# Kernel optimization log

Measured on AMD Instinct MI355X. Metric: run time of the kernel, lower is better.

## Reference

```python
import jax, jax.numpy as jnp
import numpy as np

N = 4096
D = 512
H = 3


def setup_inputs() -> dict:
    key = jax.random.key(0)
    k1, k2, k3 = jax.random.split(key, 3)
    graph_info = (jax.random.uniform(k1, (N, N)) < 0.01).astype(jnp.float32)
    h = jax.random.normal(k2, (N, D), dtype=jnp.float32)
    # xavier_normal_ with relu gain: std = sqrt(2) * sqrt(2/(fan_in+fan_out))
    std = np.sqrt(2.0) * np.sqrt(2.0 / (D + H))
    P = jax.random.normal(k3, (D, H), dtype=jnp.float32) * jnp.float32(std)
    return {"graph_info": graph_info, "h": h, "P": P}


def reference(graph_info, h, P):
    # graph_info_1 = spmm(graph_info^T, I)^T == graph_info (identity densification)
    mask = graph_info > 0                                  # [N, N]
    E = jax.nn.relu(h @ P)                                 # [N, H] per-node scores, all heads
    NEG = jnp.float32(-9e15)
    # e is broadcast along rows: att[i, j] = E[j, k] where edge (i->j) exists
    logits = jnp.where(mask[None, :, :], E.T[:, None, :], NEG)  # [H, N, N]
    att = jax.nn.softmax(logits, axis=-1)                  # row-softmax per head
    hh = jnp.einsum('hij,jd->hid', att, h)                 # [H, N, D] aggregate
    # sum_flag == 1: scale each row i by its degree (rowsum of graph_info_1)
    rowsum = jnp.sum(graph_info, axis=-1)                  # [N]
    hh = hh * rowsum[None, :, None]
    # multi_head > 1, concat=False: sum over heads
    return jnp.sum(hh, axis=0)                             # [N, D]
```

## Files before the change

### kernel.cpp

```cpp
#include <hip/hip_runtime.h>
#include <stdint.h>

#define NN 4096
#define DD 512
#define NH 3
#define WMAX 64

__device__ __forceinline__ unsigned short f2bf_rn(float x) {
    union { float f; uint32_t u; } v; v.f = x;
    uint32_t u = v.u;
    uint32_t r = (u + 0x7FFFu + ((u >> 16) & 1u)) >> 16;
    return (unsigned short)r;
}
__device__ __forceinline__ float bflo(uint32_t u) {
    union { uint32_t u; float f; } v; v.u = u << 16; return v.f;
}
__device__ __forceinline__ float bfhi(uint32_t u) {
    union { uint32_t u; float f; } v; v.u = u & 0xFFFF0000u; return v.f;
}

__global__ __launch_bounds__(256) void prep_kernel(
    const float* __restrict__ h, const float* __restrict__ P,
    float* __restrict__ w, unsigned short* __restrict__ hb)
{
    int gid = blockIdx.x * 256 + threadIdx.x;
    int row = gid >> 6, ln = gid & 63;
    const float4* h4 = (const float4*)(h + (size_t)row * DD);
    float4 va = h4[ln * 2], vb = h4[ln * 2 + 1];
    float e[8] = { va.x, va.y, va.z, va.w, vb.x, vb.y, vb.z, vb.w };

    uint32_t pk0 = (uint32_t)f2bf_rn(e[0]) | ((uint32_t)f2bf_rn(e[1]) << 16);
    uint32_t pk1 = (uint32_t)f2bf_rn(e[2]) | ((uint32_t)f2bf_rn(e[3]) << 16);
    uint32_t pk2 = (uint32_t)f2bf_rn(e[4]) | ((uint32_t)f2bf_rn(e[5]) << 16);
    uint32_t pk3 = (uint32_t)f2bf_rn(e[6]) | ((uint32_t)f2bf_rn(e[7]) << 16);
    *(uint4*)(hb + (size_t)row * DD + ln * 8) = make_uint4(pk0, pk1, pk2, pk3);

    int d0 = ln * 8;
    float a0 = 0.f, a1 = 0.f, a2 = 0.f;
    #pragma unroll
    for (int k = 0; k < 8; ++k) {
        float hv = e[k];
        const float* Pr = P + (size_t)(d0 + k) * NH;
        a0 = fmaf(hv, Pr[0], a0);
        a1 = fmaf(hv, Pr[1], a1);
        a2 = fmaf(hv, Pr[2], a2);
    }
    #pragma unroll
    for (int off = 32; off > 0; off >>= 1) {
        a0 += __shfl_down(a0, off);
        a1 += __shfl_down(a1, off);
        a2 += __shfl_down(a2, off);
    }
    if (ln == 0) {
        w[row * NH + 0] = expf(fmaxf(a0, 0.f));
        w[row * NH + 1] = expf(fmaxf(a1, 0.f));
        w[row * NH + 2] = expf(fmaxf(a2, 0.f));
    }
}

__global__ __launch_bounds__(256) void att_agg_kernel(
    const float* __restrict__ g, const unsigned short* __restrict__ hb,
    const float* __restrict__ w, float* __restrict__ out)
{
    __shared__ float s_part[4 * NH * DD];
    __shared__ int   s_list[4 * WMAX];
    __shared__ float s_z[4][NH];
    __shared__ int   s_cw[4];

    const int row = blockIdx.x, tid = threadIdx.x;
    const int wv = tid >> 6, ln = tid & 63;

    const float4* g4 = (const float4*)(g + (size_t)row * NN) + wv * 256;
    float4 v0 = g4[ln], v1 = g4[64 + ln], v2 = g4[128 + ln], v3 = g4[192 + ln];

    int* mylist = s_list + wv * WMAX;
    int cbase = wv * 1024;
    int cnt = 0;
    float4 vs[4] = { v0, v1, v2, v3 };
    #pragma unroll
    for (int k = 0; k < 4; ++k) {
        float comp[4] = { vs[k].x, vs[k].y, vs[k].z, vs[k].w };
        int col0 = cbase + k * 256 + ln * 4;
        #pragma unroll
        for (int c = 0; c < 4; ++c) {
            bool p = comp[c] > 0.f;
            unsigned long long m = __ballot(p);
            if (p) {
                unsigned pre = __builtin_amdgcn_mbcnt_lo((unsigned)m, 0u);
                pre = __builtin_amdgcn_mbcnt_hi((unsigned)(m >> 32), pre);
                int pos = cnt + (int)pre;
                if (pos < WMAX) mylist[pos] = col0 + c;
            }
            cnt += __popcll(m);
        }
    }
    if (cnt > WMAX) cnt = WMAX;

    float accA[8] = {0,0,0,0,0,0,0,0};
    float accB[8] = {0,0,0,0,0,0,0,0};
    float accC[8] = {0,0,0,0,0,0,0,0};
    float z0 = 0.f, z1 = 0.f, z2 = 0.f;
    const unsigned short* hcol = hb + ln * 8;

    if (cnt > 0) {
        int j = mylist[0];
        uint4 rn = *(const uint4*)(hcol + (size_t)j * DD);
        const float* wr = w + (size_t)j * NH;
        float wn0 = wr[0], wn1 = wr[1], wn2 = wr[2];
        for (int t = 0; t < cnt; ++t) {
            uint4 r = rn;
            float c0 = wn0, c1 = wn1, c2 = wn2;
            if (t + 1 < cnt) {
                int j2 = mylist[t + 1];
                rn = *(const uint4*)(hcol + (size_t)j2 * DD);
                const float* wr2 = w + (size_t)j2 * NH;
                wn0 = wr2[0]; wn1 = wr2[1]; wn2 = wr2[2];
            }
            z0 += c0; z1 += c1; z2 += c2;
            float e[8] = { bflo(r.x), bfhi(r.x), bflo(r.y), bfhi(r.y),
                           bflo(r.z), bfhi(r.z), bflo(r.w), bfhi(r.w) };
            #pragma unroll
            for (int q = 0; q < 8; ++q) {
                accA[q] = fmaf(c0, e[q], accA[q]);
                accB[q] = fmaf(c1, e[q], accB[q]);
                accC[q] = fmaf(c2, e[q], accC[q]);
            }
        }
    }

    {
        float* base = s_part + (wv * NH + 0) * DD + ln * 8;
        *(float4*)(base)     = make_float4(accA[0], accA[1], accA[2], accA[3]);
        *(float4*)(base + 4) = make_float4(accA[4], accA[5], accA[6], accA[7]);
        base = s_part + (wv * NH + 1) * DD + ln * 8;
        *(float4*)(base)     = make_float4(accB[0], accB[1], accB[2], accB[3]);
        *(float4*)(base + 4) = make_float4(accB[4], accB[5], accB[6], accB[7]);
        base = s_part + (wv * NH + 2) * DD + ln * 8;
        *(float4*)(base)     = make_float4(accC[0], accC[1], accC[2], accC[3]);
        *(float4*)(base + 4) = make_float4(accC[4], accC[5], accC[6], accC[7]);
    }
    if (ln == 0) { s_z[wv][0] = z0; s_z[wv][1] = z1; s_z[wv][2] = z2; s_cw[wv] = cnt; }
    __syncthreads();

    float Z0 = s_z[0][0] + s_z[1][0] + s_z[2][0] + s_z[3][0];
    float Z1 = s_z[0][1] + s_z[1][1] + s_z[2][1] + s_z[3][1];
    float Z2 = s_z[0][2] + s_z[1][2] + s_z[2][2] + s_z[3][2];
    int nnz = s_cw[0] + s_cw[1] + s_cw[2] + s_cw[3];

    int c0 = tid * 2;
    float sA0 = 0.f, sA1 = 0.f, sB0 = 0.f, sB1 = 0.f, sC0 = 0.f, sC1 = 0.f;
    #pragma unroll
    for (int W = 0; W < 4; ++W) {
        float2 pa = *(const float2*)(s_part + (W * NH + 0) * DD + c0);
        float2 pb = *(const float2*)(s_part + (W * NH + 1) * DD + c0);
        float2 pc = *(const float2*)(s_part + (W * NH + 2) * DD + c0);
        sA0 += pa.x; sA1 += pa.y;
        sB0 += pb.x; sB1 += pb.y;
        sC0 += pc.x; sC1 += pc.y;
    }
    float2 res;
    if (nnz == 0) {
        res = make_float2(0.f, 0.f);
    } else {
        float rs = (float)nnz;
        float i0 = rs / Z0, i1 = rs / Z1, i2 = rs / Z2;
        res.x = fmaf(sA0, i0, fmaf(sB0, i1, sC0 * i2));
        res.y = fmaf(sA1, i0, fmaf(sB1, i1, sC1 * i2));
    }
    ((float2*)(out + (size_t)row * DD))[tid] = res;
}

extern "C" void kernel_launch(void* const* d_in, const int* in_sizes, int n_in,
                              void* d_out, int out_size, void* d_ws, size_t ws_size,
                              hipStream_t stream) {
    const float* g = (const float*)d_in[0];
    const float* h = (const float*)d_in[1];
    const float* P = (const float*)d_in[2];
    float* out = (float*)d_out;

    float* w           = (float*)d_ws;
    unsigned short* hb = (unsigned short*)((char*)d_ws + (64 << 10));

    prep_kernel<<<(NN * 64) / 256, 256, 0, stream>>>(h, P, w, hb);
    att_agg_kernel<<<NN, 256, 0, stream>>>(g, hb, w, out);
}
```

Before: 118.0 us.

## Use nontemporal loads/stores, deepen gather prefetch, halve LDS reduction buffer

Streams the dense adjacency rows, the h input and the output through nontemporal loads and stores so they do not pollute cache meant for the gathered bf16 rows. The neighbor gather loop now prefetches two rows ahead instead of one, to hide more global-load latency. The cross-wave partial reduction uses half the LDS: waves 2-3 add into the buffers written by waves 0-1, which lowers LDS footprint and may raise occupancy but costs an extra barrier.

```diff
diff --git a/kernel.cpp b/kernel.cpp
--- a/kernel.cpp
+++ b/kernel.cpp
@@ -5,6 +5,10 @@
 #define DD 512
 #define NH 3
 #define WMAX 64
+
+typedef float        f32x4 __attribute__((ext_vector_type(4)));
+typedef float        f32x2 __attribute__((ext_vector_type(2)));
+typedef unsigned int u32x4 __attribute__((ext_vector_type(4)));
 
 __device__ __forceinline__ unsigned short f2bf_rn(float x) {
     union { float f; uint32_t u; } v; v.f = x;
@@ -25,15 +29,17 @@
 {
     int gid = blockIdx.x * 256 + threadIdx.x;
     int row = gid >> 6, ln = gid & 63;
-    const float4* h4 = (const float4*)(h + (size_t)row * DD);
-    float4 va = h4[ln * 2], vb = h4[ln * 2 + 1];
+    const f32x4* h4 = (const f32x4*)(h + (size_t)row * DD);
+    f32x4 va = __builtin_nontemporal_load(h4 + ln * 2);
+    f32x4 vb = __builtin_nontemporal_load(h4 + ln * 2 + 1);
     float e[8] = { va.x, va.y, va.z, va.w, vb.x, vb.y, vb.z, vb.w };
 
     uint32_t pk0 = (uint32_t)f2bf_rn(e[0]) | ((uint32_t)f2bf_rn(e[1]) << 16);
     uint32_t pk1 = (uint32_t)f2bf_rn(e[2]) | ((uint32_t)f2bf_rn(e[3]) << 16);
     uint32_t pk2 = (uint32_t)f2bf_rn(e[4]) | ((uint32_t)f2bf_rn(e[5]) << 16);
     uint32_t pk3 = (uint32_t)f2bf_rn(e[6]) | ((uint32_t)f2bf_rn(e[7]) << 16);
-    *(uint4*)(hb + (size_t)row * DD + ln * 8) = make_uint4(pk0, pk1, pk2, pk3);
+    u32x4 pk; pk.x = pk0; pk.y = pk1; pk.z = pk2; pk.w = pk3;
+    *(u32x4*)(hb + (size_t)row * DD + ln * 8) = pk;
 
     int d0 = ln * 8;
     float a0 = 0.f, a1 = 0.f, a2 = 0.f;
@@ -62,7 +68,7 @@
     const float* __restrict__ g, const unsigned short* __restrict__ hb,
     const float* __restrict__ w, float* __restrict__ out)
 {
-    __shared__ float s_part[4 * NH * DD];
+    __shared__ float s_part[2 * NH * DD];
     __shared__ int   s_list[4 * WMAX];
     __shared__ float s_z[4][NH];
     __shared__ int   s_cw[4];
@@ -70,13 +76,16 @@
     const int row = blockIdx.x, tid = threadIdx.x;
     const int wv = tid >> 6, ln = tid & 63;
 
-    const float4* g4 = (const float4*)(g + (size_t)row * NN) + wv * 256;
-    float4 v0 = g4[ln], v1 = g4[64 + ln], v2 = g4[128 + ln], v3 = g4[192 + ln];
+    const f32x4* g4 = (const f32x4*)(g + (size_t)row * NN) + wv * 256;
+    f32x4 v0 = __builtin_nontemporal_load(g4 + ln);
+    f32x4 v1 = __builtin_nontemporal_load(g4 + 64 + ln);
+    f32x4 v2 = __builtin_nontemporal_load(g4 + 128 + ln);
+    f32x4 v3 = __builtin_nontemporal_load(g4 + 192 + ln);
 
     int* mylist = s_list + wv * WMAX;
     int cbase = wv * 1024;
     int cnt = 0;
-    float4 vs[4] = { v0, v1, v2, v3 };
+    f32x4 vs[4] = { v0, v1, v2, v3 };
     #pragma unroll
     for (int k = 0; k < 4; ++k) {
         float comp[4] = { vs[k].x, vs[k].y, vs[k].z, vs[k].w };
@@ -102,33 +111,43 @@
     float z0 = 0.f, z1 = 0.f, z2 = 0.f;
     const unsigned short* hcol = hb + ln * 8;
 
+    u32x4 r0, r1;
+    float wa0 = 0.f, wa1 = 0.f, wa2 = 0.f, wb0 = 0.f, wb1 = 0.f, wb2 = 0.f;
     if (cnt > 0) {
         int j = mylist[0];
-        uint4 rn = *(const uint4*)(hcol + (size_t)j * DD);
+        r0 = *(const u32x4*)(hcol + (size_t)j * DD);
         const float* wr = w + (size_t)j * NH;
-        float wn0 = wr[0], wn1 = wr[1], wn2 = wr[2];
-        for (int t = 0; t < cnt; ++t) {
-            uint4 r = rn;
-            float c0 = wn0, c1 = wn1, c2 = wn2;
-            if (t + 1 < cnt) {
-                int j2 = mylist[t + 1];
-                rn = *(const uint4*)(hcol + (size_t)j2 * DD);
-                const float* wr2 = w + (size_t)j2 * NH;
-                wn0 = wr2[0]; wn1 = wr2[1]; wn2 = wr2[2];
-            }
-            z0 += c0; z1 += c1; z2 += c2;
-            float e[8] = { bflo(r.x), bfhi(r.x), bflo(r.y), bfhi(r.y),
-                           bflo(r.z), bfhi(r.z), bflo(r.w), bfhi(r.w) };
-            #pragma unroll
-            for (int q = 0; q < 8; ++q) {
-                accA[q] = fmaf(c0, e[q], accA[q]);
-                accB[q] = fmaf(c1, e[q], accB[q]);
-                accC[q] = fmaf(c2, e[q], accC[q]);
-            }
+        wa0 = wr[0]; wa1 = wr[1]; wa2 = wr[2];
+    }
+    if (cnt > 1) {
+        int j = mylist[1];
+        r1 = *(const u32x4*)(hcol + (size_t)j * DD);
+        const float* wr = w + (size_t)j * NH;
+        wb0 = wr[0]; wb1 = wr[1]; wb2 = wr[2];
+    }
+    for (int t = 0; t < cnt; ++t) {
+        u32x4 r = r0;
+        float c0 = wa0, c1 = wa1, c2 = wa2;
+        r0 = r1; wa0 = wb0; wa1 = wb1; wa2 = wb2;
+        if (t + 2 < cnt) {
+            int j2 = mylist[t + 2];
+            r1 = *(const u32x4*)(hcol + (size_t)j2 * DD);
+            const float* wr2 = w + (size_t)j2 * NH;
+            wb0 = wr2[0]; wb1 = wr2[1]; wb2 = wr2[2];
         }
-    }
-
-    {
+        z0 += c0; z1 += c1; z2 += c2;
+        float e[8] = { bflo(r.x), bfhi(r.x), bflo(r.y), bfhi(r.y),
+                       bflo(r.z), bfhi(r.z), bflo(r.w), bfhi(r.w) };
+        #pragma unroll
+        for (int q = 0; q < 8; ++q) {
+            accA[q] = fmaf(c0, e[q], accA[q]);
+            accB[q] = fmaf(c1, e[q], accB[q]);
+            accC[q] = fmaf(c2, e[q], accC[q]);
+        }
+    }
+
+    if (ln == 0) { s_z[wv][0] = z0; s_z[wv][1] = z1; s_z[wv][2] = z2; s_cw[wv] = cnt; }
+    if (wv < 2) {
         float* base = s_part + (wv * NH + 0) * DD + ln * 8;
         *(float4*)(base)     = make_float4(accA[0], accA[1], accA[2], accA[3]);
         *(float4*)(base + 4) = make_float4(accA[4], accA[5], accA[6], accA[7]);
@@ -139,7 +158,24 @@
         *(float4*)(base)     = make_float4(accC[0], accC[1], accC[2], accC[3]);
         *(float4*)(base + 4) = make_float4(accC[4], accC[5], accC[6], accC[7]);
     }
-    if (ln == 0) { s_z[wv][0] = z0; s_z[wv][1] = z1; s_z[wv][2] = z2; s_cw[wv] = cnt; }
+    __syncthreads();
+    if (wv >= 2) {
+        float* base = s_part + ((wv - 2) * NH + 0) * DD + ln * 8;
+        float4 p0 = *(float4*)(base), p1 = *(float4*)(base + 4);
+        p0.x += accA[0]; p0.y += accA[1]; p0.z += accA[2]; p0.w += accA[3];
+        p1.x += accA[4]; p1.y += accA[5]; p1.z += accA[6]; p1.w += accA[7];
+        *(float4*)(base) = p0; *(float4*)(base + 4) = p1;
+        base = s_part + ((wv - 2) * NH + 1) * DD + ln * 8;
+        p0 = *(float4*)(base); p1 = *(float4*)(base + 4);
+        p0.x += accB[0]; p0.y += accB[1]; p0.z += accB[2]; p0.w += accB[3];
+        p1.x += accB[4]; p1.y += accB[5]; p1.z += accB[6]; p1.w += accB[7];
+        *(float4*)(base) = p0; *(float4*)(base + 4) = p1;
+        base = s_part + ((wv - 2) * NH + 2) * DD + ln * 8;
+        p0 = *(float4*)(base); p1 = *(float4*)(base + 4);
+        p0.x += accC[0]; p0.y += accC[1]; p0.z += accC[2]; p0.w += accC[3];
+        p1.x += accC[4]; p1.y += accC[5]; p1.z += accC[6]; p1.w += accC[7];
+        *(float4*)(base) = p0; *(float4*)(base + 4) = p1;
+    }
     __syncthreads();
 
     float Z0 = s_z[0][0] + s_z[1][0] + s_z[2][0] + s_z[3][0];
@@ -150,7 +186,7 @@
     int c0 = tid * 2;
     float sA0 = 0.f, sA1 = 0.f, sB0 = 0.f, sB1 = 0.f, sC0 = 0.f, sC1 = 0.f;
     #pragma unroll
-    for (int W = 0; W < 4; ++W) {
+    for (int W = 0; W < 2; ++W) {
         float2 pa = *(const float2*)(s_part + (W * NH + 0) * DD + c0);
         float2 pb = *(const float2*)(s_part + (W * NH + 1) * DD + c0);
         float2 pc = *(const float2*)(s_part + (W * NH + 2) * DD + c0);
@@ -158,16 +194,16 @@
         sB0 += pb.x; sB1 += pb.y;
         sC0 += pc.x; sC1 += pc.y;
     }
-    float2 res;
+    f32x2 res;
     if (nnz == 0) {
-        res = make_float2(0.f, 0.f);
+        res.x = 0.f; res.y = 0.f;
     } else {
         float rs = (float)nnz;
         float i0 = rs / Z0, i1 = rs / Z1, i2 = rs / Z2;
         res.x = fmaf(sA0, i0, fmaf(sB0, i1, sC0 * i2));
         res.y = fmaf(sA1, i0, fmaf(sB1, i1, sC1 * i2));
     }
-    ((float2*)(out + (size_t)row * DD))[tid] = res;
+    __builtin_nontemporal_store(res, (f32x2*)(out + (size_t)row * DD) + tid);
 }
 
 extern "C" void kernel_launch(void* const* d_in, const int* in_sizes, int n_in,
```

Result: slower. 124.1 us (+5.2%).

## Move adjacency scan into prep kernel as bitmask, one wave per row in aggregation

Applied to the files above, without the earlier changes.

The dense adjacency scan now runs in the prep kernel, which compresses each row into 64 bitmask words using non-temporal loads. Those blocks run concurrently with the h-to-bf16 conversion blocks in the same launch. The aggregation kernel reads the compact bitmask and builds the neighbour list with a prefix scan, processing one row per wavefront. This removes the cross-wave shared-memory reduction and uses a two-deep prefetch of neighbour rows. The changes raise the neighbour cap to 128 and shorten the dependency chain, but each wave now walks its row's whole neighbour list serially.

```diff
diff --git a/kernel.cpp b/kernel.cpp
--- a/kernel.cpp
+++ b/kernel.cpp
@@ -4,7 +4,10 @@
 #define NN 4096
 #define DD 512
 #define NH 3
-#define WMAX 64
+#define WMAX 128
+
+typedef float        f32x4 __attribute__((ext_vector_type(4)));
+typedef unsigned int u32x4 __attribute__((ext_vector_type(4)));
 
 __device__ __forceinline__ unsigned short f2bf_rn(float x) {
     union { float f; uint32_t u; } v; v.f = x;
@@ -19,21 +22,48 @@
     union { uint32_t u; float f; } v; v.u = u & 0xFFFF0000u; return v.f;
 }
 
-__global__ __launch_bounds__(256) void prep_kernel(
-    const float* __restrict__ h, const float* __restrict__ P,
-    float* __restrict__ w, unsigned short* __restrict__ hb)
+__global__ __launch_bounds__(256) void prep_scan_kernel(
+    const float* __restrict__ g, const float* __restrict__ h,
+    const float* __restrict__ P, float* __restrict__ w,
+    unsigned short* __restrict__ hb, unsigned long long* __restrict__ bits)
 {
-    int gid = blockIdx.x * 256 + threadIdx.x;
+    const int b = blockIdx.x;
+    const int tid = threadIdx.x;
+    if (b < NN) {
+        const int row = b, wv = tid >> 6, ln = tid & 63;
+        const f32x4* g4 = (const f32x4*)(g + (size_t)row * NN);
+        f32x4 v[4];
+        #pragma unroll
+        for (int it = 0; it < 4; ++it)
+            v[it] = __builtin_nontemporal_load(g4 + it * 256 + tid);
+        #pragma unroll
+        for (int it = 0; it < 4; ++it) {
+            int chunk = it * 4 + wv;
+            unsigned long long m0 = __ballot(v[it].x > 0.f);
+            unsigned long long m1 = __ballot(v[it].y > 0.f);
+            unsigned long long m2 = __ballot(v[it].z > 0.f);
+            unsigned long long m3 = __ballot(v[it].w > 0.f);
+            if (ln < 4) {
+                unsigned long long ms = (ln == 0) ? m0 : (ln == 1) ? m1
+                                       : (ln == 2) ? m2 : m3;
+                bits[(size_t)row * 64 + chunk * 4 + ln] = ms;
+            }
+        }
+        return;
+    }
+    int gid = (b - NN) * 256 + tid;
     int row = gid >> 6, ln = gid & 63;
-    const float4* h4 = (const float4*)(h + (size_t)row * DD);
-    float4 va = h4[ln * 2], vb = h4[ln * 2 + 1];
+    const f32x4* h4 = (const f32x4*)(h + (size_t)row * DD);
+    f32x4 va = __builtin_nontemporal_load(h4 + ln * 2);
+    f32x4 vb = __builtin_nontemporal_load(h4 + ln * 2 + 1);
     float e[8] = { va.x, va.y, va.z, va.w, vb.x, vb.y, vb.z, vb.w };
 
-    uint32_t pk0 = (uint32_t)f2bf_rn(e[0]) | ((uint32_t)f2bf_rn(e[1]) << 16);
-    uint32_t pk1 = (uint32_t)f2bf_rn(e[2]) | ((uint32_t)f2bf_rn(e[3]) << 16);
-    uint32_t pk2 = (uint32_t)f2bf_rn(e[4]) | ((uint32_t)f2bf_rn(e[5]) << 16);
-    uint32_t pk3 = (uint32_t)f2bf_rn(e[6]) | ((uint32_t)f2bf_rn(e[7]) << 16);
-    *(uint4*)(hb + (size_t)row * DD + ln * 8) = make_uint4(pk0, pk1, pk2, pk3);
+    u32x4 pk;
+    pk.x = (uint32_t)f2bf_rn(e[0]) | ((uint32_t)f2bf_rn(e[1]) << 16);
+    pk.y = (uint32_t)f2bf_rn(e[2]) | ((uint32_t)f2bf_rn(e[3]) << 16);
+    pk.z = (uint32_t)f2bf_rn(e[4]) | ((uint32_t)f2bf_rn(e[5]) << 16);
+    pk.w = (uint32_t)f2bf_rn(e[6]) | ((uint32_t)f2bf_rn(e[7]) << 16);
+    *(u32x4*)(hb + (size_t)row * DD + ln * 8) = pk;
 
     int d0 = ln * 8;
     float a0 = 0.f, a1 = 0.f, a2 = 0.f;
@@ -58,43 +88,41 @@
     }
 }
 
-__global__ __launch_bounds__(256) void att_agg_kernel(
-    const float* __restrict__ g, const unsigned short* __restrict__ hb,
-    const float* __restrict__ w, float* __restrict__ out)
+__global__ __launch_bounds__(256) void agg_kernel(
+    const unsigned long long* __restrict__ bits,
+    const unsigned short* __restrict__ hb, const float* __restrict__ w,
+    float* __restrict__ out)
 {
-    __shared__ float s_part[4 * NH * DD];
-    __shared__ int   s_list[4 * WMAX];
-    __shared__ float s_z[4][NH];
-    __shared__ int   s_cw[4];
+    __shared__ int s_list[4][WMAX];
+    const int tid = threadIdx.x, wv = tid >> 6, ln = tid & 63;
+    const int row = blockIdx.x * 4 + wv;
 
-    const int row = blockIdx.x, tid = threadIdx.x;
-    const int wv = tid >> 6, ln = tid & 63;
+    unsigned long long W = bits[(size_t)row * 64 + ln];
+    int cnt = __popcll(W);
+    int inc = cnt;
+    #pragma unroll
+    for (int d = 1; d < 64; d <<= 1) {
+        int n = __shfl_up(inc, d);
+        if (ln >= d) inc += n;
+    }
+    int nnz = __shfl(inc, 63);
+    int o = inc - cnt;
+    int base_col = (ln >> 2) * 256 + (ln & 3);
+    unsigned long long Wt = W;
+    while (Wt) {
+        int bp = __builtin_ctzll(Wt); Wt &= Wt - 1;
+        if (o < WMAX) s_list[wv][o] = base_col + 4 * bp;
+        ++o;
+    }
+    __syncthreads();
 
-    const float4* g4 = (const float4*)(g + (size_t)row * NN) + wv * 256;
-    float4 v0 = g4[ln], v1 = g4[64 + ln], v2 = g4[128 + ln], v3 = g4[192 + ln];
-
-    int* mylist = s_list + wv * WMAX;
-    int cbase = wv * 1024;
-    int cnt = 0;
-    float4 vs[4] = { v0, v1, v2, v3 };
-    #pragma unroll
-    for (int k = 0; k < 4; ++k) {
-        float comp[4] = { vs[k].x, vs[k].y, vs[k].z, vs[k].w };
-        int col0 = cbase + k * 256 + ln * 4;
-        #pragma unroll
-        for (int c = 0; c < 4; ++c) {
-            bool p = comp[c] > 0.f;
-            unsigned long long m = __ballot(p);
-            if (p) {
-                unsigned pre = __builtin_amdgcn_mbcnt_lo((unsigned)m, 0u);
-                pre = __builtin_amdgcn_mbcnt_hi((unsigned)(m >> 32), pre);
-                int pos = cnt + (int)pre;
-                if (pos < WMAX) mylist[pos] = col0 + c;
-            }
-            cnt += __popcll(m);
-        }
+    float* orow = out + (size_t)row * DD + ln * 8;
+    if (nnz == 0) {
+        f32x4 z4 = {0.f, 0.f, 0.f, 0.f};
+        *(f32x4*)(orow) = z4; *(f32x4*)(orow + 4) = z4;
+        return;
     }
-    if (cnt > WMAX) cnt = WMAX;
+    int cap = nnz < WMAX ? nnz : WMAX;
 
     float accA[8] = {0,0,0,0,0,0,0,0};
     float accB[8] = {0,0,0,0,0,0,0,0};
@@ -102,72 +130,54 @@
     float z0 = 0.f, z1 = 0.f, z2 = 0.f;
     const unsigned short* hcol = hb + ln * 8;
 
-    if (cnt > 0) {
-        int j = mylist[0];
-        uint4 rn = *(const uint4*)(hcol + (size_t)j * DD);
+    u32x4 r0 = {}, r1 = {};
+    float wa0 = 0.f, wa1 = 0.f, wa2 = 0.f, wb0 = 0.f, wb1 = 0.f, wb2 = 0.f;
+    {
+        int j = s_list[wv][0];
+        r0 = *(const u32x4*)(hcol + (size_t)j * DD);
         const float* wr = w + (size_t)j * NH;
-        float wn0 = wr[0], wn1 = wr[1], wn2 = wr[2];
-        for (int t = 0; t < cnt; ++t) {
-            uint4 r = rn;
-            float c0 = wn0, c1 = wn1, c2 = wn2;
-            if (t + 1 < cnt) {
-                int j2 = mylist[t + 1];
-                rn = *(const uint4*)(hcol + (size_t)j2 * DD);
-                const float* wr2 = w + (size_t)j2 * NH;
-                wn0 = wr2[0]; wn1 = wr2[1]; wn2 = wr2[2];
-            }
-            z0 += c0; z1 += c1; z2 += c2;
-            float e[8] = { bflo(r.x), bfhi(r.x), bflo(r.y), bfhi(r.y),
-                           bflo(r.z), bfhi(r.z), bflo(r.w), bfhi(r.w) };
-            #pragma unroll
-            for (int q = 0; q < 8; ++q) {
-                accA[q] = fmaf(c0, e[q], accA[q]);
-                accB[q] = fmaf(c1, e[q], accB[q]);
-                accC[q] = fmaf(c2, e[q], accC[q]);
-            }
+        wa0 = wr[0]; wa1 = wr[1]; wa2 = wr[2];
+    }
+    if (cap > 1) {
+        int j = s_list[wv][1];
+        r1 = *(const u32x4*)(hcol + (size_t)j * DD);
+        const float* wr = w + (size_t)j * NH;
+        wb0 = wr[0]; wb1 = wr[1]; wb2 = wr[2];
+    }
+    for (int t = 0; t < cap; ++t) {
+        u32x4 r = r0;
+        float c0 = wa0, c1 = wa1, c2 = wa2;
+        r0 = r1; wa0 = wb0; wa1 = wb1; wa2 = wb2;
+        if (t + 2 < cap) {
+            int j2 = s_list[wv][t + 2];
+            r1 = *(const u32x4*)(hcol + (size_t)j2 * DD);
+            const float* wr2 = w + (size_t)j2 * NH;
+            wb0 = wr2[0]; wb1 = wr2[1]; wb2 = wr2[2];
+        }
+        z0 += c0; z1 += c1; z2 += c2;
+        float e[8] = { bflo(r.x), bfhi(r.x), bflo(r.y), bfhi(r.y),
+                       bflo(r.z), bfhi(r.z), bflo(r.w), bfhi(r.w) };
+        #pragma unroll
+        for (int q = 0; q < 8; ++q) {
+            accA[q] = fmaf(c0, e[q], accA[q]);
+            accB[q] = fmaf(c1, e[q], accB[q]);
+            accC[q] = fmaf(c2, e[q], accC[q]);
         }
     }
 
-    {
-        float* base = s_part + (wv * NH + 0) * DD + ln * 8;
-        *(float4*)(base)     = make_float4(accA[0], accA[1], accA[2], accA[3]);
-        *(float4*)(base + 4) = make_float4(accA[4], accA[5], accA[6], accA[7]);
-        base = s_part + (wv * NH + 1) * DD + ln * 8;
-        *(float4*)(base)     = make_float4(accB[0], accB[1], accB[2], accB[3]);
-        *(float4*)(base + 4) = make_float4(accB[4], accB[5], accB[6], accB[7]);
-        base = s_part + (wv * NH + 2) * DD + ln * 8;
-        *(float4*)(base)     = make_float4(accC[0], accC[1], accC[2], accC[3]);
-        *(float4*)(base + 4) = make_float4(accC[4], accC[5], accC[6], accC[7]);
-    }
-    if (ln == 0) { s_z[wv][0] = z0; s_z[wv][1] = z1; s_z[wv][2] = z2; s_cw[wv] = cnt; }
-    __syncthreads();
-
-    float Z0 = s_z[0][0] + s_z[1][0] + s_z[2][0] + s_z[3][0];
-    float Z1 = s_z[0][1] + s_z[1][1] + s_z[2][1] + s_z[3][1];
-    float Z2 = s_z[0][2] + s_z[1][2] + s_z[2][2] + s_z[3][2];
-    int nnz = s_cw[0] + s_cw[1] + s_cw[2] + s_cw[3];
-
-    int c0 = tid * 2;
-    float sA0 = 0.f, sA1 = 0.f, sB0 = 0.f, sB1 = 0.f, sC0 = 0.f, sC1 = 0.f;
-    #pragma unroll
-    for (int W = 0; W < 4; ++W) {
-        float2 pa = *(const float2*)(s_part + (W * NH + 0) * DD + c0);
-        float2 pb = *(const float2*)(s_part + (W * NH + 1) * DD + c0);
-        float2 pc = *(const float2*)(s_part + (W * NH + 2) * DD + c0);
-        sA0 += pa.x; sA1 += pa.y;
-        sB0 += pb.x; sB1 += pb.y;
-        sC0 += pc.x; sC1 += pc.y;
-    }
-    float2 res;
-    if (nnz == 0) {
-        res = make_float2(0.f, 0.f);
-    } else {
-        float rs = (float)nnz;
-        float i0 = rs / Z0, i1 = rs / Z1, i2 = rs / Z2;
-        res.x = fmaf(sA0, i0, fmaf(sB0, i1, sC0 * i2));
-        res.y = fmaf(sA1, i0, fmaf(sB1, i1, sC1 * i2));
-    }
-    ((float2*)(out + (size_t)row * DD))[tid] = res;
+    float rs = (float)nnz;
+    float i0 = rs / z0, i1 = rs / z1, i2 = rs / z2;
+    f32x4 o0, o1;
+    o0.x = fmaf(accA[0], i0, fmaf(accB[0], i1, accC[0] * i2));
+    o0.y = fmaf(accA[1], i0, fmaf(accB[1], i1, accC[1] * i2));
+    o0.z = fmaf(accA[2], i0, fmaf(accB[2], i1, accC[2] * i2));
+    o0.w = fmaf(accA[3], i0, fmaf(accB[3], i1, accC[3] * i2));
+    o1.x = fmaf(accA[4], i0, fmaf(accB[4], i1, accC[4] * i2));
+    o1.y = fmaf(accA[5], i0, fmaf(accB[5], i1, accC[5] * i2));
+    o1.z = fmaf(accA[6], i0, fmaf(accB[6], i1, accC[6] * i2));
+    o1.w = fmaf(accA[7], i0, fmaf(accB[7], i1, accC[7] * i2));
+    *(f32x4*)(orow)     = o0;
+    *(f32x4*)(orow + 4) = o1;
 }
 
 extern "C" void kernel_launch(void* const* d_in, const int* in_sizes, int n_in,
@@ -178,9 +188,10 @@
     const float* P = (const float*)d_in[2];
     float* out = (float*)d_out;
 
-    float* w           = (float*)d_ws;
-    unsigned short* hb = (unsigned short*)((char*)d_ws + (64 << 10));
+    float* w                 = (float*)d_ws;
+    unsigned long long* bits = (unsigned long long*)((char*)d_ws + (64 << 10));
+    unsigned short* hb       = (unsigned short*)((char*)d_ws + (64 << 10) + ((size_t)NN * 64 * 8));
 
-    prep_kernel<<<(NN * 64) / 256, 256, 0, stream>>>(h, P, w, hb);
-    att_agg_kernel<<<NN, 256, 0, stream>>>(g, hb, w, out);
+    prep_scan_kernel<<<NN + (NN * 64) / 256, 256, 0, stream>>>(g, h, P, w, hb, bits);
+    agg_kernel<<<NN / 4, 256, 0, stream>>>(bits, hb, w, out);
 }
```

Result: slower. 129.7 us (+9.9%).
